# Optimization experiments

Measured on AMD Instinct MI355X. Metric: run time of the kernel, lower is better.

## Reference

```python
import jax, jax.numpy as jnp
import numpy as np

N = 100000
E = 1600000
D_FEAT = 64
D_HID = 64
T = 20
DT = 0.5


def setup_inputs() -> dict:
    key = jax.random.key(0)
    ks = jax.random.split(key, 12)
    inp = {
        "S0": jax.random.uniform(ks[0], (N,), dtype=jnp.float32),
        "I0": jax.random.uniform(ks[1], (N,), dtype=jnp.float32),
        "R0": jnp.zeros((N,), dtype=jnp.float32),
        "time_grid": jnp.arange(T, dtype=jnp.float32),
        "node_feat": jax.random.normal(ks[2], (N, D_FEAT), dtype=jnp.float32),
        "edge_index": jax.random.randint(ks[3], (2, E), 0, N, dtype=jnp.int64),
        "edge_weight": jax.random.uniform(ks[4], (E,), dtype=jnp.float32),
        "W_msg": jax.random.normal(ks[5], (D_FEAT + 1, D_HID), dtype=jnp.float32) * 0.1,
        "W_self": jax.random.normal(ks[6], (D_FEAT + 1, D_HID), dtype=jnp.float32) * 0.1,
        "b_h": jnp.zeros((D_HID,), dtype=jnp.float32),
        "w_beta": jax.random.normal(ks[7], (D_HID,), dtype=jnp.float32) * 0.1,
        "b_beta": jnp.zeros((1,), dtype=jnp.float32),
        "w_gamma": jax.random.normal(ks[8], (D_HID,), dtype=jnp.float32) * 0.1,
        "b_gamma": jnp.zeros((1,), dtype=jnp.float32),
    }
    return inp


def reference(S0, I0, R0, time_grid, node_feat, edge_index, edge_weight,
              W_msg, W_self, b_h, w_beta, b_beta, w_gamma, b_gamma):
    n = S0.shape[0]
    src = edge_index[0]
    dst = edge_index[1]

    def step(carry, _):
        S, I, R = carry
        # gnn block: x_in = [node_feat, I]  -> [N, d_feat+1]
        x_in = jnp.concatenate([node_feat, I[:, None]], axis=-1)
        # project first, then gather: (x_in @ W_msg)[src] is math-equivalent to x_in[src] @ W_msg
        msg = (x_in @ W_msg)[src] * edge_weight[:, None]          # [E, d_hid]
        agg = jax.ops.segment_sum(msg, dst, num_segments=n)       # [N, d_hid]
        h = jax.nn.relu(agg + x_in @ W_self + b_h)
        # param net: per-node beta/gamma
        beta = jax.nn.sigmoid(h @ w_beta + b_beta[0])             # [N]
        gamma = jax.nn.sigmoid(h @ w_gamma + b_gamma[0])          # [N]
        # edge scatter-add force
        force = jax.ops.segment_sum(edge_weight * I[src], dst, num_segments=n)
        force = jnp.clip(force, 0.0, 1000.0)
        inf = beta * S * force
        rec = gamma * I
        S = jnp.clip(S + (-inf) * DT, 0.0, 1.0)
        I = jnp.clip(I + (inf - rec) * DT, 0.0, 1.0)
        R = jnp.clip(R + rec * DT, 0.0, 1.0)
        return (S, I, R), (I, beta, gamma)

    (_, _, _), (I_seq, betas, gammas) = jax.lax.scan(
        step, (S0, I0, R0), None, length=time_grid.shape[0])
    return I_seq, betas[-1], gammas[-1]
```

## Files before the change

### kernel.cpp

```cpp
#include <hip/hip_runtime.h>
#include <hip/hip_fp16.h>
#include <cstdint>
#include <cstddef>

#define DT_F 0.5f
#define ELL_C 64
#define NSUB 512
#define LCAP 14
#define NBIN 1024
#define NLOC_MAX 208

__global__ void detect_i64(const long long* __restrict__ ei, int E, int n,
                           int* __restrict__ flag) {
    __shared__ int ok;
    if (threadIdx.x == 0) ok = 1;
    __syncthreads();
    int m = E < 2048 ? E : 2048;
    for (int i = threadIdx.x; i < m; i += blockDim.x) {
        long long v = ei[i];
        if (v < 0 || v >= (long long)n) ok = 0;
    }
    __syncthreads();
    if (threadIdx.x == 0) flag[0] = ok;
}

__device__ __forceinline__ int ld_idx(const void* ei, size_t pos, int w64) {
    return w64 ? (int)((const long long*)ei)[pos] : ((const int*)ei)[pos];
}

__global__ void k_bin512(const void* __restrict__ ei, const float* __restrict__ ew,
                         const int* __restrict__ flag, int E, int n,
                         int colbits, float scale,
                         int2* __restrict__ staging, int scap2,
                         int* __restrict__ gcur,
                         int2* __restrict__ ovf, int* __restrict__ ovcnt, int ovcap) {
    __shared__ int2 bins[NSUB][LCAP];
    __shared__ int bcnt[NSUB];
    __shared__ int gbase[NSUB];
    int tid = threadIdx.x;
    for (int b = tid; b < NSUB; b += 256) bcnt[b] = 0;
    __syncthreads();
    int per = (E + NBIN - 1) / NBIN;
    int e0 = blockIdx.x * per;
    int e1 = e0 + per; if (e1 > E) e1 = E;
    int w64 = flag[0];
    for (int e = e0 + tid; e < e1; e += 256) {
        int d = ld_idx(ei, (size_t)E + e, w64);
        uint32_t w15 = (uint32_t)(ew[e] * scale + 0.5f);
        uint32_t sw = (w15 << colbits) | (uint32_t)ld_idx(ei, e, w64);
        int sb = (int)(((long long)d * NSUB) / n);
        int p = atomicAdd(&bcnt[sb], 1);
        if (p < LCAP) {
            bins[sb][p] = make_int2(d, (int)sw);
        } else {
            int q = atomicAdd(ovcnt, 1);
            if (q < ovcap) ovf[q] = make_int2(d, (int)sw);
        }
    }
    __syncthreads();
    for (int b = tid; b < NSUB; b += 256) {
        int c = bcnt[b]; if (c > LCAP) c = LCAP;
        bcnt[b] = c;
        gbase[b] = atomicAdd(&gcur[b], c);
    }
    __syncthreads();
    for (int b = tid; b < NSUB; b += 256) {
        int c = bcnt[b], gb = gbase[b];
        for (int i = 0; i < c; ++i) {
            int pos = gb + i;
            if (pos < scap2) {
                staging[(size_t)b * scap2 + pos] = bins[b][i];
            } else {
                int q = atomicAdd(ovcnt, 1);
                if (q < ovcap) ovf[q] = bins[b][i];
            }
        }
    }
}

__global__ void k_scatter512(const int2* __restrict__ staging, int scap2,
                             const int* __restrict__ gcur, int n,
                             int* __restrict__ cnt, uint32_t* __restrict__ ev) {
    __shared__ uint32_t lrow[NLOC_MAX * 64];
    __shared__ int lcnt[NLOC_MAX];
    int sb = blockIdx.x;
    int lo = (int)(((long long)sb * n + NSUB - 1) / NSUB);
    int hi = (int)(((long long)(sb + 1) * n + NSUB - 1) / NSUB);
    if (hi > n) hi = n;
    int nloc = hi - lo;
    int tid = threadIdx.x;
    int tot = gcur[sb]; if (tot > scap2) tot = scap2;
    if (nloc <= NLOC_MAX) {
        for (int i = tid; i < nloc; i += 256) lcnt[i] = 0;
        __syncthreads();
        for (int i = tid; i < tot; i += 256) {
            int2 t = staging[(size_t)sb * scap2 + i];
            int ni = t.x - lo;
            int p = atomicAdd(&lcnt[ni], 1);
            if (p < ELL_C) lrow[ni * 64 + p] = (uint32_t)t.y;
        }
        __syncthreads();
        for (int idx = tid; idx < nloc * 64; idx += 256) {
            int ni = idx >> 6, e = idx & 63;
            int c = lcnt[ni]; if (c > ELL_C) c = ELL_C;
            if (e < c) ev[(size_t)(lo + ni) * 64 + e] = lrow[idx];
        }
        for (int i = tid; i < nloc; i += 256) {
            int c = lcnt[i]; if (c > ELL_C) c = ELL_C;
            cnt[lo + i] = c;
        }
    } else {
        for (int i = tid; i < tot; i += 256) {
            int2 t = staging[(size_t)sb * scap2 + i];
            int p = atomicAdd(&cnt[t.x], 1);
            if (p < ELL_C) ev[(size_t)t.x * 64 + p] = (uint32_t)t.y;
        }
    }
}

__global__ void k_overflow(const int2* __restrict__ ovf, const int* __restrict__ ovcnt,
                           int ovcap, int* __restrict__ cnt, uint32_t* __restrict__ ev) {
    int tot = ovcnt[0]; if (tot > ovcap) tot = ovcap;
    for (int i = blockIdx.x * blockDim.x + threadIdx.x; i < tot;
         i += gridDim.x * blockDim.x) {
        int2 t = ovf[i];
        int p = atomicAdd(&cnt[t.x], 1);
        if (p < ELL_C) ev[(size_t)t.x * 64 + p] = (uint32_t)t.y;
    }
}

__global__ void k_h16(const float* __restrict__ x, __half* __restrict__ y, int n) {
    int i = blockIdx.x * blockDim.x + threadIdx.x;
    if (i < n) y[i] = __float2half(x[i]);
}

__global__ void proj_tiled(const float* __restrict__ nf,
                           const float* __restrict__ Wm,
                           const float* __restrict__ Wsf,
                           const float* __restrict__ bh,
                           __half* __restrict__ PMh, float* __restrict__ HC,
                           int n) {
    __shared__ float sWmT[64 * 65];
    __shared__ float sWsT[64 * 65];
    for (int i = threadIdx.x; i < 64 * 64; i += 256) {
        int k = i >> 6, j = i & 63;
        sWmT[j * 65 + k] = Wm[i];
        sWsT[j * 65 + k] = Wsf[i];
    }
    __syncthreads();
    int node0 = blockIdx.x * 64;
    int w   = threadIdx.x >> 6;
    int j   = threadIdx.x & 63;
    float accm[16], accs[16];
#pragma unroll
    for (int ni = 0; ni < 16; ++ni) { accm[ni] = 0.f; accs[ni] = 0.f; }
    for (int kq = 0; kq < 16; ++kq) {
        int k = kq * 4;
        float wm0 = sWmT[j * 65 + k],     wm1 = sWmT[j * 65 + k + 1];
        float wm2 = sWmT[j * 65 + k + 2], wm3 = sWmT[j * 65 + k + 3];
        float ws0 = sWsT[j * 65 + k],     ws1 = sWsT[j * 65 + k + 1];
        float ws2 = sWsT[j * 65 + k + 2], ws3 = sWsT[j * 65 + k + 3];
#pragma unroll
        for (int ni = 0; ni < 16; ++ni) {
            int node = node0 + w * 16 + ni;
            float4 a = make_float4(0.f, 0.f, 0.f, 0.f);
            if (node < n) a = *(const float4*)&nf[(size_t)node * 64 + k];
            accm[ni] = fmaf(a.w, wm3, fmaf(a.z, wm2, fmaf(a.y, wm1, fmaf(a.x, wm0, accm[ni]))));
            accs[ni] = fmaf(a.w, ws3, fmaf(a.z, ws2, fmaf(a.y, ws1, fmaf(a.x, ws0, accs[ni]))));
        }
    }
    float bhl = bh[j];
#pragma unroll
    for (int ni = 0; ni < 16; ++ni) {
        int node = node0 + w * 16 + ni;
        if (node < n) {
            PMh[(size_t)node * 64 + j] = __float2half(accm[ni]);
            HC[(size_t)node * 64 + j] = accs[ni] + bhl;
        }
    }
}

__global__ void edge_wide_ell(const int* __restrict__ cnt,
                              const uint32_t* __restrict__ ev,
                              const __half* __restrict__ PMh,
                              const float* __restrict__ HCin,
                              __half* __restrict__ HCh, int n,
                              int colbits, float inv_scale) {
    int wave = (blockIdx.x * blockDim.x + threadIdx.x) >> 6;
    int lane = threadIdx.x & 63;
    if (wave >= n) return;
    uint32_t cmask = (1u << colbits) - 1;
    int deg = cnt[wave]; if (deg > ELL_C) deg = ELL_C;
    int d4 = deg & ~3;
    const uint32_t* row = ev + (size_t)wave * ELL_C;
    float acc0 = 0.f, acc1 = 0.f, acc2 = 0.f, acc3 = 0.f;
    for (int e = 0; e < d4; e += 4) {
        uint4 q = *(const uint4*)&row[e];
        float v0 = __half2float(PMh[(size_t)(q.x & cmask) * 64 + lane]);
        float v1 = __half2float(PMh[(size_t)(q.y & cmask) * 64 + lane]);
        float v2 = __half2float(PMh[(size_t)(q.z & cmask) * 64 + lane]);
        float v3 = __half2float(PMh[(size_t)(q.w & cmask) * 64 + lane]);
        acc0 = fmaf((float)(q.x >> colbits) * inv_scale, v0, acc0);
        acc1 = fmaf((float)(q.y >> colbits) * inv_scale, v1, acc1);
        acc2 = fmaf((float)(q.z >> colbits) * inv_scale, v2, acc2);
        acc3 = fmaf((float)(q.w >> colbits) * inv_scale, v3, acc3);
    }
    for (int e = d4; e < deg; ++e) {
        uint32_t q = row[e];
        acc0 = fmaf((float)(q >> colbits) * inv_scale,
                    __half2float(PMh[(size_t)(q & cmask) * 64 + lane]), acc0);
    }
    size_t o = (size_t)wave * 64 + lane;
    HCh[o] = __float2half(HCin[o] + ((acc0 + acc1) + (acc2 + acc3)));
}

__global__ void step_fused4(const int* __restrict__ cnt,
                            const uint32_t* __restrict__ ev,
                            const __half2* __restrict__ HCh2,
                            const float4* __restrict__ wmL4,
                            const float4* __restrict__ wsL4,
                            const float4* __restrict__ wb4, const float* __restrict__ bb,
                            const float4* __restrict__ wg4, const float* __restrict__ bg,
                            const float* __restrict__ I_old,
                            const __half* __restrict__ Ih_old,
                            __half* __restrict__ Ih_new,
                            float* __restrict__ S,
                            float* __restrict__ Iseq_t,
                            float* __restrict__ beta_out, float* __restrict__ gamma_out,
                            int n, int last, int colbits, float inv_scale) {
    int wid  = (blockIdx.x * blockDim.x + threadIdx.x) >> 6;
    int lane = threadIdx.x & 63;
    int l16  = lane & 15;
    int node = wid * 4 + (lane >> 4);
    if (node >= n) return;
    uint32_t cmask = (1u << colbits) - 1;
    int deg = cnt[node]; if (deg > ELL_C) deg = ELL_C;
    const uint32_t* row = ev + (size_t)node * ELL_C;
    float f = 0.f;
    for (int e = l16; e < deg; e += 16) {
        uint32_t p = row[e];
        f = fmaf((float)(p >> colbits) * inv_scale,
                 __half2float(Ih_old[p & cmask]), f);
    }
    f += __shfl_xor(f, 1); f += __shfl_xor(f, 2);
    f += __shfl_xor(f, 4); f += __shfl_xor(f, 8);
    float Iv = I_old[node];
    __half2 hA = HCh2[(size_t)node * 32 + l16 * 2];
    __half2 hB = HCh2[(size_t)node * 32 + l16 * 2 + 1];
    float2 fA = __half22float2(hA);
    float2 fB = __half22float2(hB);
    float4 wm = wmL4[l16], wsv = wsL4[l16];
    float4 h;
    h.x = fmaxf(fmaf(f, wm.x, fmaf(Iv, wsv.x, fA.x)), 0.f);
    h.y = fmaxf(fmaf(f, wm.y, fmaf(Iv, wsv.y, fA.y)), 0.f);
    h.z = fmaxf(fmaf(f, wm.z, fmaf(Iv, wsv.z, fB.x)), 0.f);
    h.w = fmaxf(fmaf(f, wm.w, fmaf(Iv, wsv.w, fB.y)), 0.f);
    float4 wbv = wb4[l16], wgv = wg4[l16];
    float pb = fmaf(h.x, wbv.x, fmaf(h.y, wbv.y, fmaf(h.z, wbv.z, h.w * wbv.w)));
    float pg = fmaf(h.x, wgv.x, fmaf(h.y, wgv.y, fmaf(h.z, wgv.z, h.w * wgv.w)));
    pb += __shfl_xor(pb, 1); pg += __shfl_xor(pg, 1);
    pb += __shfl_xor(pb, 2); pg += __shfl_xor(pg, 2);
    pb += __shfl_xor(pb, 4); pg += __shfl_xor(pg, 4);
    pb += __shfl_xor(pb, 8); pg += __shfl_xor(pg, 8);
    if (l16 == 0) {
        float beta  = 1.f / (1.f + expf(-(pb + bb[0])));
        float gamma = 1.f / (1.f + expf(-(pg + bg[0])));
        float fc = fminf(fmaxf(f, 0.f), 1000.f);
        float Sv = S[node];
        float inf_ = beta * Sv * fc;
        float rec  = gamma * Iv;
        float Sn = fminf(fmaxf(Sv - inf_ * DT_F, 0.f), 1.f);
        float In = fminf(fmaxf(Iv + (inf_ - rec) * DT_F, 0.f), 1.f);
        S[node] = Sn;
        Iseq_t[node] = In;
        Ih_new[node] = __float2half(In);
        if (last) { beta_out[node] = beta; gamma_out[node] = gamma; }
    }
}

extern "C" void kernel_launch(void* const* d_in, const int* in_sizes, int n_in,
                              void* d_out, int out_size, void* d_ws, size_t ws_size,
                              hipStream_t stream) {
    const float* S0  = (const float*)d_in[0];
    const float* I0  = (const float*)d_in[1];
    const float* nf  = (const float*)d_in[4];
    const void*  ei  = d_in[5];
    const float* ew  = (const float*)d_in[6];
    const float* Wm  = (const float*)d_in[7];
    const float* Wsf = (const float*)d_in[8];
    const float* bh  = (const float*)d_in[9];
    const float* wb  = (const float*)d_in[10];
    const float* bb  = (const float*)d_in[11];
    const float* wg  = (const float*)d_in[12];
    const float* bg  = (const float*)d_in[13];

    const int n = in_sizes[0];
    const int T = in_sizes[3];
    const int E = in_sizes[6];

    int colbits = 1;
    while ((1 << colbits) < n) ++colbits;
    float scale = (float)((1u << (32 - colbits)) - 1);
    float inv_scale = 1.0f / scale;
    const int scap2 = E / NSUB + E / (NSUB * 4) + 256;
    const int ovcap = E;

    char* ws = (char*)d_ws;
    size_t off = 0;
    auto alloc = [&](size_t bytes) {
        size_t p = off;
        off = (off + bytes + 255) & ~(size_t)255;
        return p;
    };
    float*  HC      = (float*)(ws + alloc((size_t)n * 64 * 4));
    __half* PMh     = (__half*)(ws + alloc((size_t)n * 64 * 2));
    __half* HCh     = (__half*)(ws + alloc((size_t)n * 64 * 2));
    float*  S       = (float*)(ws + alloc((size_t)n * 4));
    __half* Ih0     = (__half*)(ws + alloc((size_t)n * 2));
    __half* IhA     = (__half*)(ws + alloc((size_t)n * 2));
    __half* IhB     = (__half*)(ws + alloc((size_t)n * 2));
    int*    cnt     = (int*)(ws + alloc((size_t)n * 4));
    uint32_t* ev    = (uint32_t*)(ws + alloc((size_t)n * ELL_C * 4));
    int2*   staging = (int2*)(ws + alloc((size_t)NSUB * scap2 * 8));
    int2*   ovf     = (int2*)(ws + alloc((size_t)ovcap * 8));
    int*    gcur    = (int*)(ws + alloc((size_t)NSUB * 4));
    int*    ovcnt   = (int*)(ws + alloc(256));
    int*    flag    = (int*)(ws + alloc(256));
    if (off > ws_size) return;

    float* out       = (float*)d_out;
    float* beta_out  = out + (size_t)T * n;
    float* gamma_out = out + (size_t)T * n + n;

    hipMemcpyAsync(S, S0, (size_t)n * 4, hipMemcpyDeviceToDevice, stream);
    hipMemsetAsync(cnt, 0, (size_t)n * 4, stream);
    hipMemsetAsync(gcur, 0, (size_t)NSUB * 4, stream);
    hipMemsetAsync(ovcnt, 0, 256, stream);

    detect_i64<<<1, 256, 0, stream>>>((const long long*)ei, E, n, flag);
    k_bin512<<<NBIN, 256, 0, stream>>>(ei, ew, flag, E, n, colbits, scale,
                                       staging, scap2, gcur, ovf, ovcnt, ovcap);
    k_scatter512<<<NSUB, 256, 0, stream>>>(staging, scap2, gcur, n, cnt, ev);
    k_overflow<<<64, 256, 0, stream>>>(ovf, ovcnt, ovcap, cnt, ev);
    k_h16<<<(n + 255) / 256, 256, 0, stream>>>(I0, Ih0, n);

    proj_tiled<<<(n + 63) / 64, 256, 0, stream>>>(nf, Wm, Wsf, bh, PMh, HC, n);
    edge_wide_ell<<<(n * 64 + 255) / 256, 256, 0, stream>>>(
        cnt, ev, PMh, HC, HCh, n, colbits, inv_scale);

    const __half2* HCh2 = (const __half2*)HCh;
    const float4* wmL4 = (const float4*)(Wm  + 64 * 64);
    const float4* wsL4 = (const float4*)(Wsf + 64 * 64);
    const float4* wb4  = (const float4*)wb;
    const float4* wg4  = (const float4*)wg;
    int swaves = (n + 3) / 4;
    int sblocks = (swaves * 64 + 255) / 256;
    for (int t = 0; t < T; ++t) {
        const float*  Iold = (t == 0) ? I0 : out + (size_t)(t - 1) * n;
        const __half* Ihp  = (t == 0) ? Ih0 : ((t & 1) ? IhA : IhB);
        __half*       Ihc  = (t & 1) ? IhB : IhA;
        step_fused4<<<sblocks, 256, 0, stream>>>(
            cnt, ev, HCh2, wmL4, wsL4, wb4, bb, wg4, bg,
            Iold, Ihp, Ihc, S, out + (size_t)t * n, beta_out, gamma_out,
            n, t == T - 1 ? 1 : 0, colbits, inv_scale);
    }
}
```

Baseline: 477.7 us.

## Use fp16 MFMA for node projection and unroll edge gather by eight

The scalar fp32 tiled projection of node features through W_msg and W_self is replaced by a matrix-core kernel using 16x16x32 fp16 MFMA, with the weights pre-swizzled into shared memory in fragment layout. The ELL edge aggregation loop is unrolled to eight edges per iteration so more independent gathers are in flight. The projection now rounds inputs to fp16, which loses some precision, and output stores become strided per row. Both kernels run once in setup, outside the time loop, so their share of total time is limited.

```diff
diff --git a/kernel.cpp b/kernel.cpp
--- a/kernel.cpp
+++ b/kernel.cpp
@@ -9,6 +9,9 @@
 #define LCAP 14
 #define NBIN 1024
 #define NLOC_MAX 208
+
+typedef _Float16 f16x8 __attribute__((ext_vector_type(8)));
+typedef float f32x4 __attribute__((ext_vector_type(4)));
 
 __global__ void detect_i64(const long long* __restrict__ ei, int E, int n,
                            int* __restrict__ flag) {
@@ -134,48 +137,68 @@
     if (i < n) y[i] = __float2half(x[i]);
 }
 
-__global__ void proj_tiled(const float* __restrict__ nf,
-                           const float* __restrict__ Wm,
-                           const float* __restrict__ Wsf,
-                           const float* __restrict__ bh,
-                           __half* __restrict__ PMh, float* __restrict__ HC,
-                           int n) {
-    __shared__ float sWmT[64 * 65];
-    __shared__ float sWsT[64 * 65];
-    for (int i = threadIdx.x; i < 64 * 64; i += 256) {
-        int k = i >> 6, j = i & 63;
-        sWmT[j * 65 + k] = Wm[i];
-        sWsT[j * 65 + k] = Wsf[i];
-    }
-    __syncthreads();
-    int node0 = blockIdx.x * 64;
-    int w   = threadIdx.x >> 6;
-    int j   = threadIdx.x & 63;
-    float accm[16], accs[16];
+__global__ void proj_mfma(const float* __restrict__ nf,
+                          const float* __restrict__ Wm,
+                          const float* __restrict__ Wsf,
+                          const float* __restrict__ bh,
+                          __half* __restrict__ PMh, float* __restrict__ HC,
+                          int n) {
+    __shared__ _Float16 sW[2][8][512];
+    int tid = threadIdx.x;
+    for (int idx = tid; idx < 8192; idx += 256) {
+        int m   = idx >> 12;
+        int rem = idx & 4095;
+        int f   = rem >> 9;
+        int ln  = (rem >> 3) & 63;
+        int el  = rem & 7;
+        int ks = f >> 2, jt = f & 3;
+        int k = ks * 32 + (ln >> 4) * 8 + el;
+        int j = jt * 16 + (ln & 15);
+        const float* W = m ? Wsf : Wm;
+        sW[m][f][ln * 8 + el] = (_Float16)W[k * 64 + j];
+    }
+    __syncthreads();
+    int w = tid >> 6, l = tid & 63;
+    int kg = l >> 4;
+    int node0 = blockIdx.x * 64 + w * 16;
+    int nodeA = node0 + (l & 15);
+    f16x8 a0 = {}, a1 = {};
+    if (nodeA < n) {
+        const float* p = nf + (size_t)nodeA * 64 + kg * 8;
+        float4 u0 = *(const float4*)(p);
+        float4 u1 = *(const float4*)(p + 4);
+        float4 v0 = *(const float4*)(p + 32);
+        float4 v1 = *(const float4*)(p + 36);
+        a0[0]=(_Float16)u0.x; a0[1]=(_Float16)u0.y; a0[2]=(_Float16)u0.z; a0[3]=(_Float16)u0.w;
+        a0[4]=(_Float16)u1.x; a0[5]=(_Float16)u1.y; a0[6]=(_Float16)u1.z; a0[7]=(_Float16)u1.w;
+        a1[0]=(_Float16)v0.x; a1[1]=(_Float16)v0.y; a1[2]=(_Float16)v0.z; a1[3]=(_Float16)v0.w;
+        a1[4]=(_Float16)v1.x; a1[5]=(_Float16)v1.y; a1[6]=(_Float16)v1.z; a1[7]=(_Float16)v1.w;
+    }
+    f32x4 accm[4], accs[4];
 #pragma unroll
-    for (int ni = 0; ni < 16; ++ni) { accm[ni] = 0.f; accs[ni] = 0.f; }
-    for (int kq = 0; kq < 16; ++kq) {
-        int k = kq * 4;
-        float wm0 = sWmT[j * 65 + k],     wm1 = sWmT[j * 65 + k + 1];
-        float wm2 = sWmT[j * 65 + k + 2], wm3 = sWmT[j * 65 + k + 3];
-        float ws0 = sWsT[j * 65 + k],     ws1 = sWsT[j * 65 + k + 1];
-        float ws2 = sWsT[j * 65 + k + 2], ws3 = sWsT[j * 65 + k + 3];
+    for (int jt = 0; jt < 4; ++jt) { accm[jt] = (f32x4){0.f,0.f,0.f,0.f};
+                                     accs[jt] = (f32x4){0.f,0.f,0.f,0.f}; }
 #pragma unroll
-        for (int ni = 0; ni < 16; ++ni) {
-            int node = node0 + w * 16 + ni;
-            float4 a = make_float4(0.f, 0.f, 0.f, 0.f);
-            if (node < n) a = *(const float4*)&nf[(size_t)node * 64 + k];
-            accm[ni] = fmaf(a.w, wm3, fmaf(a.z, wm2, fmaf(a.y, wm1, fmaf(a.x, wm0, accm[ni]))));
-            accs[ni] = fmaf(a.w, ws3, fmaf(a.z, ws2, fmaf(a.y, ws1, fmaf(a.x, ws0, accs[ni]))));
-        }
-    }
-    float bhl = bh[j];
+    for (int jt = 0; jt < 4; ++jt) {
+        f16x8 bm0 = *(const f16x8*)&sW[0][jt][l * 8];
+        f16x8 bm1 = *(const f16x8*)&sW[0][4 + jt][l * 8];
+        accm[jt] = __builtin_amdgcn_mfma_f32_16x16x32_f16(a0, bm0, accm[jt], 0, 0, 0);
+        accm[jt] = __builtin_amdgcn_mfma_f32_16x16x32_f16(a1, bm1, accm[jt], 0, 0, 0);
+        f16x8 bs0 = *(const f16x8*)&sW[1][jt][l * 8];
+        f16x8 bs1 = *(const f16x8*)&sW[1][4 + jt][l * 8];
+        accs[jt] = __builtin_amdgcn_mfma_f32_16x16x32_f16(a0, bs0, accs[jt], 0, 0, 0);
+        accs[jt] = __builtin_amdgcn_mfma_f32_16x16x32_f16(a1, bs1, accs[jt], 0, 0, 0);
+    }
 #pragma unroll
-    for (int ni = 0; ni < 16; ++ni) {
-        int node = node0 + w * 16 + ni;
+    for (int r = 0; r < 4; ++r) {
+        int node = node0 + kg * 4 + r;
         if (node < n) {
-            PMh[(size_t)node * 64 + j] = __float2half(accm[ni]);
-            HC[(size_t)node * 64 + j] = accs[ni] + bhl;
+#pragma unroll
+            for (int jt = 0; jt < 4; ++jt) {
+                int j = jt * 16 + (l & 15);
+                PMh[(size_t)node * 64 + j] = __float2half(accm[jt][r]);
+                HC[(size_t)node * 64 + j] = accs[jt][r] + bh[j];
+            }
         }
     }
 }
@@ -191,11 +214,32 @@
     if (wave >= n) return;
     uint32_t cmask = (1u << colbits) - 1;
     int deg = cnt[wave]; if (deg > ELL_C) deg = ELL_C;
+    int d8 = deg & ~7;
     int d4 = deg & ~3;
     const uint32_t* row = ev + (size_t)wave * ELL_C;
     float acc0 = 0.f, acc1 = 0.f, acc2 = 0.f, acc3 = 0.f;
-    for (int e = 0; e < d4; e += 4) {
-        uint4 q = *(const uint4*)&row[e];
+    for (int e = 0; e < d8; e += 8) {
+        uint4 qa = *(const uint4*)&row[e];
+        uint4 qb = *(const uint4*)&row[e + 4];
+        float v0 = __half2float(PMh[(size_t)(qa.x & cmask) * 64 + lane]);
+        float v1 = __half2float(PMh[(size_t)(qa.y & cmask) * 64 + lane]);
+        float v2 = __half2float(PMh[(size_t)(qa.z & cmask) * 64 + lane]);
+        float v3 = __half2float(PMh[(size_t)(qa.w & cmask) * 64 + lane]);
+        float v4 = __half2float(PMh[(size_t)(qb.x & cmask) * 64 + lane]);
+        float v5 = __half2float(PMh[(size_t)(qb.y & cmask) * 64 + lane]);
+        float v6 = __half2float(PMh[(size_t)(qb.z & cmask) * 64 + lane]);
+        float v7 = __half2float(PMh[(size_t)(qb.w & cmask) * 64 + lane]);
+        acc0 = fmaf((float)(qa.x >> colbits) * inv_scale, v0, acc0);
+        acc1 = fmaf((float)(qa.y >> colbits) * inv_scale, v1, acc1);
+        acc2 = fmaf((float)(qa.z >> colbits) * inv_scale, v2, acc2);
+        acc3 = fmaf((float)(qa.w >> colbits) * inv_scale, v3, acc3);
+        acc0 = fmaf((float)(qb.x >> colbits) * inv_scale, v4, acc0);
+        acc1 = fmaf((float)(qb.y >> colbits) * inv_scale, v5, acc1);
+        acc2 = fmaf((float)(qb.z >> colbits) * inv_scale, v6, acc2);
+        acc3 = fmaf((float)(qb.w >> colbits) * inv_scale, v7, acc3);
+    }
+    if (d8 < d4) {
+        uint4 q = *(const uint4*)&row[d8];
         float v0 = __half2float(PMh[(size_t)(q.x & cmask) * 64 + lane]);
         float v1 = __half2float(PMh[(size_t)(q.y & cmask) * 64 + lane]);
         float v2 = __half2float(PMh[(size_t)(q.z & cmask) * 64 + lane]);
@@ -344,7 +388,7 @@
     k_overflow<<<64, 256, 0, stream>>>(ovf, ovcnt, ovcap, cnt, ev);
     k_h16<<<(n + 255) / 256, 256, 0, stream>>>(I0, Ih0, n);
 
-    proj_tiled<<<(n + 63) / 64, 256, 0, stream>>>(nf, Wm, Wsf, bh, PMh, HC, n);
+    proj_mfma<<<(n + 63) / 64, 256, 0, stream>>>(nf, Wm, Wsf, bh, PMh, HC, n);
     edge_wide_ell<<<(n * 64 + 255) / 256, 256, 0, stream>>>(
         cnt, ev, PMh, HC, HCh, n, colbits, inv_scale);
 
```

Measured after the change: 429.3 us, median of 2. 1.11x faster.
